# Kernel optimization log

Measured on AMD Instinct MI355X. Metric: run time of the kernel, lower is better.

Reference implementation:

```python
import jax, jax.numpy as jnp
import numpy as np

NEIGHBOR_RATE = 0.1  # neighbor_rate init arg
LEAKY_SLOPE = 0.2
NEG_INF = -1.0e9


def setup_inputs() -> dict:
    key = jax.random.key(0)
    k1, k2, k3, k4 = jax.random.split(key, 4)
    B, N, Din, H, hd = 4, 2048, 128, 4, 32  # output_dim = H*hd = 128
    h = jax.random.normal(k1, (B, N, Din), jnp.float32)
    adj = jax.random.uniform(k2, (B, N, N), jnp.float32)
    # stacked per-head params: W[k] in [Din, hd], a[k] in [2*hd]
    w_bound = 1.0 / np.sqrt(Din)
    a_bound = 1.0 / np.sqrt(2 * hd)
    W = jax.random.uniform(k3, (H, Din, hd), jnp.float32, -w_bound, w_bound)
    a = jax.random.uniform(k4, (H, 2 * hd), jnp.float32, -a_bound, a_bound)
    return {"h": h, "adj": adj, "W": W, "a": a}


def reference(h, adj, W, a):
    B, N, _ = h.shape
    H, _, hd = W.shape
    k = int(NEIGHBOR_RATE * N)  # num_neighbors
    # Wh: [B,H,N,hd]
    Wh = jnp.einsum('bnf,hfd->bhnd', h, W)
    # cat([Wh_i, Wh_j]) @ a  ==  Wh_i @ a[:hd] + Wh_j @ a[hd:] (broadcast trick)
    s_i = jnp.einsum('bhnd,hd->bhn', Wh, a[:, :hd])
    s_j = jnp.einsum('bhnd,hd->bhn', Wh, a[:, hd:])
    e = jax.nn.leaky_relu(s_i[..., :, None] + s_j[..., None, :], LEAKY_SLOPE)  # [B,H,N,N]
    # top-k mask along last (neighbor) axis, built by scatter like torch .scatter_
    _, idx = jax.lax.top_k(e, k)  # [B,H,N,k]
    row_mask = lambda i: jnp.zeros((N,), jnp.bool_).at[i].set(True)
    mask = jax.vmap(row_mask)(idx.reshape(-1, k)).reshape(e.shape)
    masked = jnp.where(mask, e, NEG_INF)
    attn = jax.nn.softmax(masked, axis=-1) * adj[:, None]  # [B,H,N,N]
    hp = jnp.einsum('bhnm,bhmd->bhnd', attn, Wh)
    # concat heads on feature dim -> [B,N,H*hd]
    return hp.transpose(0, 2, 1, 3).reshape(B, N, H * hd)
```

## Files before the change

### kernel.cpp

```cpp
#include <hip/hip_runtime.h>
#include <hip/hip_bf16.h>
#include <cmath>

#define BB 4
#define NN 2048
#define DIN 128
#define HH 4
#define HD 32
#define KSEL 204
#define BH (BB*HH)
#define KPAD 256
#define KST 264

typedef __attribute__((ext_vector_type(8))) short short8;
typedef __attribute__((ext_vector_type(4))) short short4v;
typedef __attribute__((ext_vector_type(4))) float float4v;

static __device__ inline short f2bf(float x) {
    __hip_bfloat16 b = __float2bfloat16(x);
    return __builtin_bit_cast(short, b);
}

typedef __attribute__((address_space(1))) const unsigned gq_t;
typedef __attribute__((address_space(3))) unsigned lq_t;
static __device__ inline void gload_lds16(const void* g, void* l) {
    __builtin_amdgcn_global_load_lds((gq_t*)g, (lq_t*)l, 16, 0, 0);
}

__global__ __launch_bounds__(256) void s_kernel(const float* __restrict__ h,
                                                const float* __restrict__ W,
                                                const float* __restrict__ a,
                                                float* __restrict__ si, float* __restrict__ sj) {
    __shared__ float w1L[HH][DIN], w2L[HH][DIN];
    int t = threadIdx.x;
    for (int e = t; e < 8 * DIN; e += 256) {
        int f = e & 127, v = e >> 7;
        int hh = v >> 1, half = v & 1;
        const float* Wp = W + ((size_t)hh * DIN + f) * HD;
        const float* ap = a + hh * 64 + half * 32;
        float acc = 0.f;
#pragma unroll
        for (int d = 0; d < 32; ++d) acc += Wp[d] * ap[d];
        if (half == 0) w1L[hh][f] = acc; else w2L[hh][f] = acc;
    }
    __syncthreads();

    int gid = blockIdx.x * 256 + t;
    int row = gid >> 2;
    int q   = gid & 3;
    int b = row >> 11, n = row & 2047;
    const float* hr = h + (size_t)row * DIN;

    float s1h0 = 0.f, s1h1 = 0.f, s1h2 = 0.f, s1h3 = 0.f;
    float s2h0 = 0.f, s2h1 = 0.f, s2h2 = 0.f, s2h3 = 0.f;
#pragma unroll
    for (int i = 0; i < 8; ++i) {
        int f = q * 4 + i * 16;
        float4 x = *(const float4*)(hr + f);
        const float* wa0 = &w1L[0][f]; const float* wb0 = &w2L[0][f];
        const float* wa1 = &w1L[1][f]; const float* wb1 = &w2L[1][f];
        const float* wa2 = &w1L[2][f]; const float* wb2 = &w2L[2][f];
        const float* wa3 = &w1L[3][f]; const float* wb3 = &w2L[3][f];
        s1h0 += x.x*wa0[0] + x.y*wa0[1] + x.z*wa0[2] + x.w*wa0[3];
        s2h0 += x.x*wb0[0] + x.y*wb0[1] + x.z*wb0[2] + x.w*wb0[3];
        s1h1 += x.x*wa1[0] + x.y*wa1[1] + x.z*wa1[2] + x.w*wa1[3];
        s2h1 += x.x*wb1[0] + x.y*wb1[1] + x.z*wb1[2] + x.w*wb1[3];
        s1h2 += x.x*wa2[0] + x.y*wa2[1] + x.z*wa2[2] + x.w*wa2[3];
        s2h2 += x.x*wb2[0] + x.y*wb2[1] + x.z*wb2[2] + x.w*wb2[3];
        s1h3 += x.x*wa3[0] + x.y*wa3[1] + x.z*wa3[2] + x.w*wa3[3];
        s2h3 += x.x*wb3[0] + x.y*wb3[1] + x.z*wb3[2] + x.w*wb3[3];
    }
#pragma unroll
    for (int off = 1; off <= 2; off <<= 1) {
        s1h0 += __shfl_xor(s1h0, off); s2h0 += __shfl_xor(s2h0, off);
        s1h1 += __shfl_xor(s1h1, off); s2h1 += __shfl_xor(s2h1, off);
        s1h2 += __shfl_xor(s1h2, off); s2h2 += __shfl_xor(s2h2, off);
        s1h3 += __shfl_xor(s1h3, off); s2h3 += __shfl_xor(s2h3, off);
    }
    float o1 = (q == 0) ? s1h0 : (q == 1) ? s1h1 : (q == 2) ? s1h2 : s1h3;
    float o2 = (q == 0) ? s2h0 : (q == 1) ? s2h1 : (q == 2) ? s2h2 : s2h3;
    size_t o = (size_t)(b * HH + q) * NN + n;
    si[o] = o1; sj[o] = o2;
}

__global__ __launch_bounds__(1024) void select_kernel(
        const float* __restrict__ h, const float* __restrict__ W,
        const float* __restrict__ sj,
        int* __restrict__ idxsel, float* __restrict__ sjsel,
        float* __restrict__ sjmax, short* __restrict__ Whsel) {
    int bh = blockIdx.x;
    int b = bh >> 2, hh = bh & 3;
    int t = threadIdx.x, lane = t & 63, w = t >> 6;
    __shared__ float sv[NN];
    __shared__ short WT[32][136];
    __shared__ int hist16[16][256];
    __shared__ int binInfo[2];
    __shared__ int wtot[4];
    __shared__ int wtotg[16], wtote[16], woffg[16], woffe[16];
    __shared__ float wmax[16];
    __shared__ int idxLDS[KSEL];

    for (int e = t; e < 32 * 128; e += 1024) {
        int n = e & 31, k = e >> 5;
        WT[n][k] = f2bf(W[(size_t)hh * (DIN * HD) + k * HD + n]);
    }

    const float* s = sj + (size_t)bh * NN;
    int j0 = t * 2;
    float2 xx = *(const float2*)(s + j0);
    sv[j0] = xx.x; sv[j0 + 1] = xx.y;
    unsigned u0 = __builtin_bit_cast(unsigned, xx.x);
    unsigned u1 = __builtin_bit_cast(unsigned, xx.y);
    u0 = (u0 & 0x80000000u) ? ~u0 : (u0 | 0x80000000u);
    u1 = (u1 & 0x80000000u) ? ~u1 : (u1 | 0x80000000u);
    float lmax = fmaxf(xx.x, xx.y);
#pragma unroll
    for (int off = 32; off >= 1; off >>= 1) lmax = fmaxf(lmax, __shfl_xor(lmax, off));
    if (lane == 0) wmax[w] = lmax;
    __syncthreads();
    if (t == 0) {
        float m = wmax[0];
#pragma unroll
        for (int i = 1; i < 16; ++i) m = fmaxf(m, wmax[i]);
        sjmax[bh] = m;
    }

    unsigned prefix = 0;
    int need = KSEL;
#pragma unroll
    for (int shift = 24; shift >= 0; shift -= 8) {
        ((int*)hist16)[t] = 0; ((int*)hist16)[t + 1024] = 0;
        ((int*)hist16)[t + 2048] = 0; ((int*)hist16)[t + 3072] = 0;
        __syncthreads();
        unsigned hmask = (shift < 24) ? (0xFFFFFFFFu << (shift + 8)) : 0u;
        if (((u0 ^ prefix) & hmask) == 0) atomicAdd(&hist16[w][(u0 >> shift) & 255], 1);
        if (((u1 ^ prefix) & hmask) == 0) atomicAdd(&hist16[w][(u1 >> shift) & 255], 1);
        __syncthreads();
        int sc = 0, hv = 0, bb = 0;
        if (t < 256) {
            bb = 255 - t;
            hv = 0;
#pragma unroll
            for (int i = 0; i < 16; ++i) hv += hist16[i][bb];
            sc = hv;
#pragma unroll
            for (int off = 1; off < 64; off <<= 1) {
                int u = __shfl_up(sc, off);
                if (lane >= off) sc += u;
            }
            if (lane == 63) wtot[w] = sc;
        }
        __syncthreads();
        if (t < 256) {
            int woffset = 0;
#pragma unroll
            for (int i = 0; i < 4; ++i) woffset += (i < w) ? wtot[i] : 0;
            int incl = sc + woffset;
            int excl = incl - hv;
            if (incl >= need && excl < need) {
                binInfo[0] = bb;
                binInfo[1] = excl;
            }
        }
        __syncthreads();
        prefix |= ((unsigned)binInfo[0]) << shift;
        need -= binInfo[1];
        __syncthreads();
    }
    unsigned T = prefix;
    int n_gt = KSEL - need;

    int cg = (u0 > T ? 1 : 0) + (u1 > T ? 1 : 0);
    int ce = (u0 == T ? 1 : 0) + (u1 == T ? 1 : 0);
    int sg = cg, se = ce;
#pragma unroll
    for (int off = 1; off < 64; off <<= 1) {
        int ug = __shfl_up(sg, off), ue = __shfl_up(se, off);
        if (lane >= off) { sg += ug; se += ue; }
    }
    if (lane == 63) { wtotg[w] = sg; wtote[w] = se; }
    __syncthreads();
    if (t == 0) {
        int rg = 0, re = 0;
#pragma unroll
        for (int i = 0; i < 16; ++i) {
            woffg[i] = rg; rg += wtotg[i];
            woffe[i] = re; re += wtote[i];
        }
    }
    __syncthreads();
    int pg = woffg[w] + sg - cg;
    int te = woffe[w] + se - ce;
    {
        unsigned kk[2] = {u0, u1};
#pragma unroll
        for (int r = 0; r < 2; ++r) {
            int j = j0 + r;
            if (kk[r] > T) {
                idxsel[bh * KSEL + pg] = j;
                sjsel[bh * KSEL + pg] = sv[j];
                idxLDS[pg] = j;
                pg++;
            } else if (kk[r] == T) {
                if (te < need) {
                    int pos = n_gt + te;
                    idxsel[bh * KSEL + pos] = j;
                    sjsel[bh * KSEL + pos] = sv[j];
                    idxLDS[pos] = j;
                }
                te++;
            }
        }
    }
    __syncthreads();

    {
        int mr = lane & 15, quad = lane >> 4;
        int jjp = w * 16 + mr;
        bool valid = jjp < KSEL;
        const float* hrow = h + ((size_t)b * NN + (valid ? idxLDS[jjp] : 0)) * DIN + quad * 8;
        float4v acc0 = {0.f, 0.f, 0.f, 0.f};
        float4v acc1 = {0.f, 0.f, 0.f, 0.f};
#pragma unroll
        for (int ks = 0; ks < 4; ++ks) {
            short8 afr;
            if (valid) {
                float4 xa = *(const float4*)(hrow + ks * 32);
                float4 xb = *(const float4*)(hrow + ks * 32 + 4);
                afr[0] = f2bf(xa.x); afr[1] = f2bf(xa.y); afr[2] = f2bf(xa.z); afr[3] = f2bf(xa.w);
                afr[4] = f2bf(xb.x); afr[5] = f2bf(xb.y); afr[6] = f2bf(xb.z); afr[7] = f2bf(xb.w);
            } else {
                afr = (short8){0, 0, 0, 0, 0, 0, 0, 0};
            }
            short8 b0 = *(const short8*)&WT[mr][ks * 32 + quad * 8];
            short8 b1 = *(const short8*)&WT[16 + mr][ks * 32 + quad * 8];
            acc0 = __builtin_amdgcn_mfma_f32_16x16x32_bf16(afr, b0, acc0, 0, 0, 0);
            acc1 = __builtin_amdgcn_mfma_f32_16x16x32_bf16(afr, b1, acc1, 0, 0, 0);
        }
        short4v o0, o1;
#pragma unroll
        for (int r = 0; r < 4; ++r) { o0[r] = f2bf(acc0[r]); o1[r] = f2bf(acc1[r]); }
        size_t base = (size_t)bh * HD * KPAD;
        int jjs = w * 16 + quad * 4;
        *(short4v*)&Whsel[base + (size_t)mr * KPAD + jjs] = o0;
        *(short4v*)&Whsel[base + (size_t)(16 + mr) * KPAD + jjs] = o1;
    }
}

__global__ __launch_bounds__(256) void attn2_kernel(
        const float* __restrict__ adj, const float* __restrict__ si,
        const int* __restrict__ idxsel, const float* __restrict__ sjsel,
        const float* __restrict__ sjmax, const short* __restrict__ Whsel,
        float* __restrict__ out) {
    int b = blockIdx.x >> 7;
    int tile = blockIdx.x & 127;
    __shared__ float adjbuf[2][2][NN];
    __shared__ short PSb[HH][16][KST];
    __shared__ int   idxS[HH][KPAD];
    __shared__ float sjS[HH][KPAD];
    __shared__ float invZS[HH][16];
    __shared__ float smaxS[HH];
    int t = threadIdx.x, w = t >> 6, lane = t & 63;
    int mr = lane & 15, quad = lane >> 4;

    int i0 = tile * 16;
    const float* adjb = adj + (size_t)b * NN * NN + (size_t)i0 * NN;

    for (int e = t; e < HH * KPAD; e += 256) {
        int hh = e >> 8, jj = e & 255;
        bool v = jj < KSEL;
        idxS[hh][jj] = v ? idxsel[(b * HH + hh) * KSEL + jj] : 0;
        sjS[hh][jj]  = v ? sjsel[(b * HH + hh) * KSEL + jj] : -1e30f;
    }
    if (t < HH) smaxS[t] = sjmax[b * HH + t];

    short8 bfr[2][8];
    {
        const short* wp = Whsel + (size_t)((b * HH + w) * HD) * KPAD;
#pragma unroll
        for (int ni = 0; ni < 2; ++ni)
#pragma unroll
            for (int ks = 0; ks < 8; ++ks)
                bfr[ni][ks] = *(const short8*)(wp + (size_t)(ni * 16 + mr) * KPAD + ks * 32 + quad * 8);
    }
    int bh = b * HH + w;
    float sivAll = (lane < 16) ? si[(size_t)bh * NN + i0 + lane] : 0.f;

    __syncthreads();

    {
        int lx = lane << 4;
#pragma unroll
        for (int q = 0; q < 4; ++q) {
            int off = (q << 12) + (w << 10);
            gload_lds16((const char*)adjb + off + lx, (char*)&adjbuf[0][0][0] + off);
        }
        const char* gs1 = (const char*)(adjb + (size_t)2 * NN);
#pragma unroll
        for (int q = 0; q < 4; ++q) {
            int off = (q << 12) + (w << 10);
            gload_lds16(gs1 + off + lx, (char*)&adjbuf[1][0][0] + off);
        }
    }
    asm volatile("s_waitcnt vmcnt(4)" ::: "memory");
    __builtin_amdgcn_sched_barrier(0);
    __builtin_amdgcn_s_barrier();

    float smax = smaxS[w];
    for (int s = 0; s < 8; ++s) {
        int cur = s & 1;
        if (s >= 1 && s < 7) {
            const char* gs = (const char*)(adjb + (size_t)((s + 1) * 2) * NN);
            char* lb = (char*)&adjbuf[cur ^ 1][0][0];
            int lx = lane << 4;
#pragma unroll
            for (int q = 0; q < 4; ++q) {
                int off = (q << 12) + (w << 10);
                gload_lds16(gs + off + lx, lb + off);
            }
        }
#pragma unroll
        for (int r = 0; r < 2; ++r) {
            int i_loc = s * 2 + r;
            float siv = __shfl(sivAll, i_loc);
            float m = siv + smax;
            m = (m >= 0.f) ? m : 0.2f * m;
            float z = 0.f;
            short* prow = &PSb[w][i_loc][0];
#pragma unroll
            for (int k = 0; k < 2; ++k) {
                int jj = k * 128 + lane * 2;
                int ja = idxS[w][jj], jb = idxS[w][jj + 1];
                float ava = adjbuf[cur][r][ja], avb = adjbuf[cur][r][jb];
                float ea = siv + sjS[w][jj];
                float eb = siv + sjS[w][jj + 1];
                ea = (ea >= 0.f) ? ea : 0.2f * ea;
                eb = (eb >= 0.f) ? eb : 0.2f * eb;
                float ca = __expf(ea - m);
                float cb = __expf(eb - m);
                z += ca + cb;
                short2 p;
                p.x = f2bf(ca * ava);
                p.y = f2bf(cb * avb);
                *(short2*)&prow[jj] = p;
            }
#pragma unroll
            for (int off = 32; off >= 1; off >>= 1) z += __shfl_xor(z, off);
            if (lane == 0) invZS[w][i_loc] = 1.0f / z;
        }
        if (s < 7) {
            asm volatile("s_waitcnt vmcnt(0)" ::: "memory");
            __builtin_amdgcn_sched_barrier(0);
            __builtin_amdgcn_s_barrier();
        }
    }
#pragma unroll
    for (int ni = 0; ni < 2; ++ni) {
        float4v acc = {0.f, 0.f, 0.f, 0.f};
#pragma unroll
        for (int ks = 0; ks < 8; ++ks) {
            short8 afr = *(const short8*)&PSb[w][mr][ks * 32 + quad * 8];
            acc = __builtin_amdgcn_mfma_f32_16x16x32_bf16(afr, bfr[ni][ks], acc, 0, 0, 0);
        }
#pragma unroll
        for (int r = 0; r < 4; ++r) {
            int i_loc = quad * 4 + r;
            int d = ni * 16 + mr;
            out[((size_t)(b * NN + i0 + i_loc)) * (HH * HD) + w * HD + d] =
                acc[r] * invZS[w][i_loc];
        }
    }
}

extern "C" void kernel_launch(void* const* d_in, const int* in_sizes, int n_in,
                              void* d_out, int out_size, void* d_ws, size_t ws_size,
                              hipStream_t stream) {
    const float* h   = (const float*)d_in[0];
    const float* adj = (const float*)d_in[1];
    const float* W   = (const float*)d_in[2];
    const float* a   = (const float*)d_in[3];
    float* out = (float*)d_out;

    float* si     = (float*)d_ws;
    float* sj     = si + (size_t)BH * NN;
    float* sjsel  = sj + (size_t)BH * NN;
    float* sjmax  = sjsel + (size_t)BH * KSEL;
    int*   idxsel = (int*)(sjmax + 16);
    short* Whsel  = (short*)(idxsel + (size_t)BH * KSEL);

    s_kernel<<<128, 256, 0, stream>>>(h, W, a, si, sj);
    select_kernel<<<BH, 1024, 0, stream>>>(h, W, sj, idxsel, sjsel, sjmax, Whsel);
    attn2_kernel<<<BB * 128, 256, 0, stream>>>(adj, si, idxsel, sjsel, sjmax, Whsel, out);
}
```

Measured before the change: 128.9 us.

## Split attn2 work across 8 waves: two waves per head sharing rows and output halves

Doubles attn2 block size to 512 threads so each head gets two waves. Each wave handles one of the two rows per pipeline stage and one 16-column half of the output MFMA. Each wave now issues fewer adjacency loads and holds fewer B-fragment registers, which is meant to raise latency hiding and occupancy on a kernel bound by memory latency. A full block barrier is added before the MFMA stage because rows written by one wave are now read by its partner.

```diff
diff --git a/kernel.cpp b/kernel.cpp
--- a/kernel.cpp
+++ b/kernel.cpp
@@ -247,7 +247,7 @@
     }
 }
 
-__global__ __launch_bounds__(256) void attn2_kernel(
+__global__ __launch_bounds__(512) void attn2_kernel(
         const float* __restrict__ adj, const float* __restrict__ si,
         const int* __restrict__ idxsel, const float* __restrict__ sjsel,
         const float* __restrict__ sjmax, const short* __restrict__ Whsel,
@@ -260,80 +260,68 @@
     __shared__ float sjS[HH][KPAD];
     __shared__ float invZS[HH][16];
     __shared__ float smaxS[HH];
-    int t = threadIdx.x, w = t >> 6, lane = t & 63;
+    int t = threadIdx.x, w8 = t >> 6, lane = t & 63;
+    int hh = w8 >> 1, g = w8 & 1;
     int mr = lane & 15, quad = lane >> 4;
 
     int i0 = tile * 16;
-    const float* adjb = adj + (size_t)b * NN * NN + (size_t)i0 * NN;
-
-    for (int e = t; e < HH * KPAD; e += 256) {
-        int hh = e >> 8, jj = e & 255;
+    const char* adjb = (const char*)(adj + (size_t)b * NN * NN + (size_t)i0 * NN);
+
+    for (int e = t; e < HH * KPAD; e += 512) {
+        int h2 = e >> 8, jj = e & 255;
         bool v = jj < KSEL;
-        idxS[hh][jj] = v ? idxsel[(b * HH + hh) * KSEL + jj] : 0;
-        sjS[hh][jj]  = v ? sjsel[(b * HH + hh) * KSEL + jj] : -1e30f;
+        idxS[h2][jj] = v ? idxsel[(b * HH + h2) * KSEL + jj] : 0;
+        sjS[h2][jj]  = v ? sjsel[(b * HH + h2) * KSEL + jj] : -1e30f;
     }
     if (t < HH) smaxS[t] = sjmax[b * HH + t];
 
-    short8 bfr[2][8];
-    {
-        const short* wp = Whsel + (size_t)((b * HH + w) * HD) * KPAD;
-#pragma unroll
-        for (int ni = 0; ni < 2; ++ni)
-#pragma unroll
-            for (int ks = 0; ks < 8; ++ks)
-                bfr[ni][ks] = *(const short8*)(wp + (size_t)(ni * 16 + mr) * KPAD + ks * 32 + quad * 8);
-    }
-    int bh = b * HH + w;
-    float sivAll = (lane < 16) ? si[(size_t)bh * NN + i0 + lane] : 0.f;
-
-    __syncthreads();
-
-    {
-        int lx = lane << 4;
-#pragma unroll
-        for (int q = 0; q < 4; ++q) {
-            int off = (q << 12) + (w << 10);
-            gload_lds16((const char*)adjb + off + lx, (char*)&adjbuf[0][0][0] + off);
-        }
-        const char* gs1 = (const char*)(adjb + (size_t)2 * NN);
-#pragma unroll
-        for (int q = 0; q < 4; ++q) {
-            int off = (q << 12) + (w << 10);
-            gload_lds16(gs1 + off + lx, (char*)&adjbuf[1][0][0] + off);
-        }
-    }
-    asm volatile("s_waitcnt vmcnt(4)" ::: "memory");
+    short8 bfr[8];
+    {
+        const short* wp = Whsel + (size_t)((b * HH + hh) * HD) * KPAD;
+#pragma unroll
+        for (int ks = 0; ks < 8; ++ks)
+            bfr[ks] = *(const short8*)(wp + (size_t)(g * 16 + mr) * KPAD + ks * 32 + quad * 8);
+    }
+    int bh = b * HH + hh;
+    float sivAll = (lane < 8) ? si[(size_t)bh * NN + i0 + 2 * lane + g] : 0.f;
+
+    __syncthreads();
+
+    {
+        int lx = lane << 4, off = w8 << 10;
+        gload_lds16(adjb + off + lx,              (char*)&adjbuf[0][0][0] + off);
+        gload_lds16(adjb + 8192 + off + lx,       (char*)&adjbuf[0][0][0] + 8192 + off);
+        gload_lds16(adjb + 16384 + off + lx,      (char*)&adjbuf[1][0][0] + off);
+        gload_lds16(adjb + 24576 + off + lx,      (char*)&adjbuf[1][0][0] + 8192 + off);
+    }
+    asm volatile("s_waitcnt vmcnt(2)" ::: "memory");
     __builtin_amdgcn_sched_barrier(0);
     __builtin_amdgcn_s_barrier();
 
-    float smax = smaxS[w];
+    float smax = smaxS[hh];
     for (int s = 0; s < 8; ++s) {
         int cur = s & 1;
         if (s >= 1 && s < 7) {
-            const char* gs = (const char*)(adjb + (size_t)((s + 1) * 2) * NN);
+            const char* gs = adjb + (size_t)(s + 1) * 16384;
             char* lb = (char*)&adjbuf[cur ^ 1][0][0];
-            int lx = lane << 4;
-#pragma unroll
-            for (int q = 0; q < 4; ++q) {
-                int off = (q << 12) + (w << 10);
-                gload_lds16(gs + off + lx, lb + off);
-            }
-        }
-#pragma unroll
-        for (int r = 0; r < 2; ++r) {
-            int i_loc = s * 2 + r;
-            float siv = __shfl(sivAll, i_loc);
+            int lx = lane << 4, off = w8 << 10;
+            gload_lds16(gs + off + lx,        lb + off);
+            gload_lds16(gs + 8192 + off + lx, lb + 8192 + off);
+        }
+        {
+            int i_loc = 2 * s + g;
+            float siv = __shfl(sivAll, s);
             float m = siv + smax;
             m = (m >= 0.f) ? m : 0.2f * m;
             float z = 0.f;
-            short* prow = &PSb[w][i_loc][0];
+            short* prow = &PSb[hh][i_loc][0];
 #pragma unroll
             for (int k = 0; k < 2; ++k) {
                 int jj = k * 128 + lane * 2;
-                int ja = idxS[w][jj], jb = idxS[w][jj + 1];
-                float ava = adjbuf[cur][r][ja], avb = adjbuf[cur][r][jb];
-                float ea = siv + sjS[w][jj];
-                float eb = siv + sjS[w][jj + 1];
+                int ja = idxS[hh][jj], jb = idxS[hh][jj + 1];
+                float ava = adjbuf[cur][g][ja], avb = adjbuf[cur][g][jb];
+                float ea = siv + sjS[hh][jj];
+                float eb = siv + sjS[hh][jj + 1];
                 ea = (ea >= 0.f) ? ea : 0.2f * ea;
                 eb = (eb >= 0.f) ? eb : 0.2f * eb;
                 float ca = __expf(ea - m);
@@ -346,7 +334,7 @@
             }
 #pragma unroll
             for (int off = 32; off >= 1; off >>= 1) z += __shfl_xor(z, off);
-            if (lane == 0) invZS[w][i_loc] = 1.0f / z;
+            if (lane == 0) invZS[hh][i_loc] = 1.0f / z;
         }
         if (s < 7) {
             asm volatile("s_waitcnt vmcnt(0)" ::: "memory");
@@ -354,20 +342,21 @@
             __builtin_amdgcn_s_barrier();
         }
     }
-#pragma unroll
-    for (int ni = 0; ni < 2; ++ni) {
+    __syncthreads();
+
+    {
         float4v acc = {0.f, 0.f, 0.f, 0.f};
 #pragma unroll
         for (int ks = 0; ks < 8; ++ks) {
-            short8 afr = *(const short8*)&PSb[w][mr][ks * 32 + quad * 8];
-            acc = __builtin_amdgcn_mfma_f32_16x16x32_bf16(afr, bfr[ni][ks], acc, 0, 0, 0);
+            short8 afr = *(const short8*)&PSb[hh][mr][ks * 32 + quad * 8];
+            acc = __builtin_amdgcn_mfma_f32_16x16x32_bf16(afr, bfr[ks], acc, 0, 0, 0);
         }
 #pragma unroll
         for (int r = 0; r < 4; ++r) {
             int i_loc = quad * 4 + r;
-            int d = ni * 16 + mr;
-            out[((size_t)(b * NN + i0 + i_loc)) * (HH * HD) + w * HD + d] =
-                acc[r] * invZS[w][i_loc];
+            int d = g * 16 + mr;
+            out[((size_t)(b * NN + i0 + i_loc)) * (HH * HD) + hh * HD + d] =
+                acc[r] * invZS[hh][i_loc];
         }
     }
 }
@@ -390,5 +379,5 @@
 
     s_kernel<<<128, 256, 0, stream>>>(h, W, a, si, sj);
     select_kernel<<<BH, 1024, 0, stream>>>(h, W, sj, idxsel, sjsel, sjmax, Whsel);
-    attn2_kernel<<<BB * 128, 256, 0, stream>>>(adj, si, idxsel, sjsel, sjmax, Whsel, out);
-}
+    attn2_kernel<<<BB * 128, 512, 0, stream>>>(adj, si, idxsel, sjsel, sjmax, Whsel, out);
+}
```

After: 126.5 us. Within noise of the previous version (-1.9%).
